# Performance work log

Hardware: AMD Instinct MI355X
Metric: run time of the kernel (lower is better)

Reference implementation:

```python
import jax, jax.numpy as jnp
import numpy as np

D_MODEL = 512
NUM_HEADS = 8
D_K = D_MODEL // NUM_HEADS
DIM_FF = 2048
EPS = 1e-5


def layer_norm(x, gamma, beta):
    mu = jnp.mean(x, axis=-1, keepdims=True)
    var = jnp.mean(jnp.square(x - mu), axis=-1, keepdims=True)
    return (x - mu) * jax.lax.rsqrt(var + EPS) * gamma + beta


def setup_inputs() -> dict:
    key = jax.random.key(0)
    ks = jax.random.split(key, 10)
    B, L = 8, 1024
    s = 1.0 / np.sqrt(D_MODEL)
    return {
        "h": jax.random.normal(ks[0], (B, L, D_MODEL), jnp.float32),
        "attn_bias": jax.random.normal(ks[1], (B, NUM_HEADS, L, L), jnp.float32),
        "mask": jnp.ones((B, L), jnp.int32),
        "Wqkv": jax.random.normal(ks[2], (D_MODEL, 3 * D_MODEL), jnp.float32) * s,
        "bqkv": jnp.zeros((3 * D_MODEL,), jnp.float32),
        "Wo": jax.random.normal(ks[3], (D_MODEL, D_MODEL), jnp.float32) * s,
        "bo": jnp.zeros((D_MODEL,), jnp.float32),
        "W1": jax.random.normal(ks[4], (D_MODEL, DIM_FF), jnp.float32) * s,
        "b1": jnp.zeros((DIM_FF,), jnp.float32),
        "W2": jax.random.normal(ks[5], (DIM_FF, D_MODEL), jnp.float32) * (1.0 / np.sqrt(DIM_FF)),
        "b2": jnp.zeros((D_MODEL,), jnp.float32),
        "g1": jnp.ones((D_MODEL,), jnp.float32),
        "be1": jnp.zeros((D_MODEL,), jnp.float32),
        "g2": jnp.ones((D_MODEL,), jnp.float32),
        "be2": jnp.zeros((D_MODEL,), jnp.float32),
    }


def reference(h, attn_bias, mask, Wqkv, bqkv, Wo, bo, W1, b1, W2, b2, g1, be1, g2, be2):
    B, L, D = h.shape
    H, dk = NUM_HEADS, D_K
    qkv = h @ Wqkv + bqkv                      # [B, L, 3D]
    q, k, v = jnp.split(qkv, 3, axis=-1)
    q = q.reshape(B, L, H, dk).transpose(0, 2, 1, 3)  # [B, H, L, dk]
    k = k.reshape(B, L, H, dk).transpose(0, 2, 1, 3)
    v = v.reshape(B, L, H, dk).transpose(0, 2, 1, 3)
    scores = jnp.einsum('bhqd,bhkd->bhqk', q, k) / np.sqrt(dk)
    scores = scores + attn_bias
    scores = jnp.where(mask[:, None, None, :] > 0, scores, -jnp.inf)
    attn = jax.nn.softmax(scores, axis=-1)
    out = jnp.einsum('bhqk,bhkd->bhqd', attn, v)       # [B, H, L, dk]
    out = out.transpose(0, 2, 1, 3).reshape(B, L, D)
    out = out @ Wo + bo
    h = layer_norm(h + out, g1, be1)
    ff = jax.nn.relu(h @ W1 + b1) @ W2 + b2
    h = layer_norm(h + ff, g2, be2)
    return h
```

## Files before the change

kernel.cpp:

```cpp
#include <hip/hip_runtime.h>
#include <hip/hip_bf16.h>
#include <math.h>

#define NUM_HEADS 8
#define SEQ_L 1024
#define EPS 1e-5f
#define KVBLK 64
#define LOG2E 1.44269504088896f

typedef __bf16 bf16x8 __attribute__((ext_vector_type(8)));
typedef float f32x4 __attribute__((ext_vector_type(4)));
typedef __hip_bfloat16 bf16;

#define AS1 __attribute__((address_space(1)))
#define AS3 __attribute__((address_space(3)))

__device__ __forceinline__ void gload_lds16(const void* g, void* l) {
    __builtin_amdgcn_global_load_lds((const AS1 unsigned*)g, (AS3 unsigned*)l, 16, 0, 0);
}

__device__ __forceinline__ unsigned short bfb(float x) {
    bf16 b = __float2bfloat16(x);
    return *(unsigned short*)&b;
}

__device__ __forceinline__ int swz64(int el, int row) { return el ^ ((row & 7) << 3); }

__global__ __launch_bounds__(256) void f32_to_bf16_kernel(
    const float* __restrict__ in, bf16* __restrict__ out, int n)
{
    const int i = (blockIdx.x * 256 + threadIdx.x) * 4;
    if (i >= n) return;
    const float4 v = *(const float4*)&in[i];
    out[i + 0] = __float2bfloat16(v.x);
    out[i + 1] = __float2bfloat16(v.y);
    out[i + 2] = __float2bfloat16(v.z);
    out[i + 3] = __float2bfloat16(v.w);
}

__global__ __launch_bounds__(256) void transpose_w(
    const float* __restrict__ W, bf16* __restrict__ Wt, int K, int N)
{
    __shared__ float t[32][33];
    const int tx = threadIdx.x & 31, ty = threadIdx.x >> 5;
    const int n0 = blockIdx.x * 32, k0 = blockIdx.y * 32;
    #pragma unroll
    for (int r = 0; r < 4; ++r)
        t[ty + 8 * r][tx] = W[(size_t)(k0 + ty + 8 * r) * N + n0 + tx];
    __syncthreads();
    #pragma unroll
    for (int r = 0; r < 4; ++r)
        Wt[(size_t)(n0 + ty + 8 * r) * K + k0 + tx] = __float2bfloat16(t[tx][ty + 8 * r]);
}

__global__ __launch_bounds__(256) void gemm_bf16(
    const bf16* __restrict__ A, const bf16* __restrict__ Bt,
    const float* __restrict__ bias,
    float* __restrict__ C, bf16* __restrict__ Cb,
    int M, int N, int K, int relu)
{
    __shared__ __align__(16) bf16 Abuf[128 * 32];
    __shared__ __align__(16) bf16 Bbuf[128 * 32];
    const int tid = threadIdx.x;
    const int wv = tid >> 6, lane = tid & 63;
    const int row0 = blockIdx.y * 128, col0 = blockIdx.x * 128;
    const int wm = (wv >> 1) * 64, wn = (wv & 1) * 64;
    const int r0 = lane & 15, kb = lane >> 4;

    f32x4 acc[4][4] = {};
    const int arow = lane >> 2;
    const int akoff = (lane & 3) * 8;

    for (int k0 = 0; k0 < K; k0 += 32) {
        #pragma unroll
        for (int s = 0; s < 2; ++s) {
            const int c = 2 * wv + s;
            gload_lds16(&A[(size_t)(row0 + c * 16 + arow) * K + k0 + akoff], &Abuf[c * 512]);
            gload_lds16(&Bt[(size_t)(col0 + c * 16 + arow) * K + k0 + akoff], &Bbuf[c * 512]);
        }
        __syncthreads();

        bf16x8 a[4], b[4];
        #pragma unroll
        for (int i = 0; i < 4; ++i)
            a[i] = *(const bf16x8*)&Abuf[(wm + i * 16 + r0) * 32 + kb * 8];
        #pragma unroll
        for (int j = 0; j < 4; ++j)
            b[j] = *(const bf16x8*)&Bbuf[(wn + j * 16 + r0) * 32 + kb * 8];
        #pragma unroll
        for (int i = 0; i < 4; ++i)
            #pragma unroll
            for (int j = 0; j < 4; ++j)
                acc[i][j] = __builtin_amdgcn_mfma_f32_16x16x32_bf16(a[i], b[j], acc[i][j], 0, 0, 0);
        __syncthreads();
    }

    float bv[4];
    #pragma unroll
    for (int j = 0; j < 4; ++j) bv[j] = bias[col0 + wn + j * 16 + r0];

    #pragma unroll
    for (int i = 0; i < 4; ++i) {
        #pragma unroll
        for (int j = 0; j < 4; ++j) {
            const int col = col0 + wn + j * 16 + r0;
            #pragma unroll
            for (int reg = 0; reg < 4; ++reg) {
                const int row = row0 + wm + i * 16 + kb * 4 + reg;
                float v = acc[i][j][reg] + bv[j];
                if (relu) v = fmaxf(v, 0.f);
                if (C)  C[(size_t)row * N + col] = v;
                if (Cb) Cb[(size_t)row * N + col] = __float2bfloat16(v);
            }
        }
    }
}

__global__ __launch_bounds__(256) void gemm_qkv(
    const bf16* __restrict__ A, const bf16* __restrict__ Bt,
    const float* __restrict__ bias,
    bf16* __restrict__ Qb, bf16* __restrict__ Kb, bf16* __restrict__ Vtb,
    int M, int N, int K)
{
    __shared__ __align__(16) bf16 Abuf[128 * 32];
    __shared__ __align__(16) bf16 Bbuf[128 * 32];
    const int tid = threadIdx.x;
    const int wv = tid >> 6, lane = tid & 63;
    const int row0 = blockIdx.y * 128, col0 = blockIdx.x * 128;
    const int wm = (wv >> 1) * 64, wn = (wv & 1) * 64;
    const int r0 = lane & 15, kb = lane >> 4;

    f32x4 acc[4][4] = {};
    const int arow = lane >> 2;
    const int akoff = (lane & 3) * 8;

    for (int k0 = 0; k0 < K; k0 += 32) {
        #pragma unroll
        for (int s = 0; s < 2; ++s) {
            const int c = 2 * wv + s;
            gload_lds16(&A[(size_t)(row0 + c * 16 + arow) * K + k0 + akoff], &Abuf[c * 512]);
            gload_lds16(&Bt[(size_t)(col0 + c * 16 + arow) * K + k0 + akoff], &Bbuf[c * 512]);
        }
        __syncthreads();

        bf16x8 a[4], b[4];
        #pragma unroll
        for (int i = 0; i < 4; ++i)
            a[i] = *(const bf16x8*)&Abuf[(wm + i * 16 + r0) * 32 + kb * 8];
        #pragma unroll
        for (int j = 0; j < 4; ++j)
            b[j] = *(const bf16x8*)&Bbuf[(wn + j * 16 + r0) * 32 + kb * 8];
        #pragma unroll
        for (int i = 0; i < 4; ++i)
            #pragma unroll
            for (int j = 0; j < 4; ++j)
                acc[i][j] = __builtin_amdgcn_mfma_f32_16x16x32_bf16(a[i], b[j], acc[i][j], 0, 0, 0);
        __syncthreads();
    }

    #pragma unroll
    for (int i = 0; i < 4; ++i) {
        #pragma unroll
        for (int j = 0; j < 4; ++j) {
            const int col = col0 + wn + j * 16 + r0;
            const float bv = bias[col];
            const int region = col >> 9;
            const int cc = col & 511;
            const int head = cc >> 6, d = cc & 63;
            const int l0 = row0 + wm + i * 16 + kb * 4;
            const int b_ = l0 >> 10, l_ = l0 & 1023;
            if (region == 2) {
                unsigned short pk[4];
                #pragma unroll
                for (int reg = 0; reg < 4; ++reg) pk[reg] = bfb(acc[i][j][reg] + bv);
                *(ushort4*)&Vtb[((size_t)(b_ * NUM_HEADS + head) * 64 + d) * SEQ_L + l_] =
                    make_ushort4(pk[0], pk[1], pk[2], pk[3]);
            } else {
                const float s = (region == 0) ? (0.125f * LOG2E) : 1.0f;
                bf16* dst = (region == 0) ? Qb : Kb;
                #pragma unroll
                for (int reg = 0; reg < 4; ++reg) {
                    dst[((size_t)(b_ * NUM_HEADS + head) * SEQ_L + l_ + reg) * 64 + d] =
                        __float2bfloat16((acc[i][j][reg] + bv) * s);
                }
            }
        }
    }
}

__global__ __launch_bounds__(256) void attn_mfma(
    const bf16* __restrict__ Qb, const bf16* __restrict__ Kb,
    const bf16* __restrict__ Vtb, const float* __restrict__ abias,
    const int* __restrict__ mask, bf16* __restrict__ out)
{
    const int bh = blockIdx.y;
    const int b = bh >> 3, h = bh & 7;
    const int q0 = blockIdx.x * 64;
    const int tid = threadIdx.x;
    const int wv = tid >> 6, lane = tid & 63;
    const int ql = lane & 15;
    const int hi = lane >> 4;

    __shared__ __align__(16) bf16 Ks[KVBLK * 64];
    __shared__ __align__(16) bf16 Vs[64 * KVBLK];
    __shared__ __align__(16) bf16 Ps[4][16 * 64];
    __shared__ __align__(16) float biasL[4][16 * 64];
    __shared__ float maskf[KVBLK];

    const int qrow = q0 + wv * 16 + ql;
    bf16x8 qf[2];
    #pragma unroll
    for (int kk = 0; kk < 2; ++kk)
        qf[kk] = *(const bf16x8*)&Qb[((size_t)bh * SEQ_L + qrow) * 64 + kk * 32 + hi * 8];

    const int sr = tid >> 3;
    const int sc8 = (tid & 7) * 8;
    const int br = lane >> 4;
    const int bc = (lane & 15) * 4;

    f32x4 o[4] = {};
    float m = -1e30f, l = 0.f;
    const size_t bias_base = ((size_t)(b * NUM_HEADS + h) * SEQ_L + q0 + wv * 16) * SEQ_L;

    bf16x8 kreg[2], vreg[2];
    f32x4 breg[4];
    float mreg = 0.f;
    #pragma unroll
    for (int it = 0; it < 2; ++it) {
        const int row = sr + it * 32;
        kreg[it] = *(const bf16x8*)&Kb[((size_t)bh * SEQ_L + row) * 64 + sc8];
        vreg[it] = *(const bf16x8*)&Vtb[((size_t)bh * 64 + row) * SEQ_L + sc8];
    }
    #pragma unroll
    for (int s = 0; s < 4; ++s)
        breg[s] = *(const f32x4*)&abias[bias_base + (size_t)(s * 4 + br) * SEQ_L + bc];
    if (tid < KVBLK) mreg = (mask[b * SEQ_L + tid] > 0) ? 0.f : -1e30f;

    for (int k0 = 0; k0 < SEQ_L; k0 += KVBLK) {
        __syncthreads();

        #pragma unroll
        for (int it = 0; it < 2; ++it) {
            const int row = sr + it * 32;
            *(bf16x8*)&Ks[swz64(row * 64 + sc8, row)] = kreg[it];
            *(bf16x8*)&Vs[swz64(row * 64 + sc8, row)] = vreg[it];
        }
        if (tid < KVBLK) maskf[tid] = mreg;
        #pragma unroll
        for (int s = 0; s < 4; ++s) {
            const int row = s * 4 + br;
            const int q = (bc >> 2) ^ (row & 7);
            *(f32x4*)&biasL[wv][row * 64 + q * 4] = breg[s];
        }
        __syncthreads();

        const int k1 = k0 + KVBLK;
        if (k1 < SEQ_L) {
            #pragma unroll
            for (int it = 0; it < 2; ++it) {
                const int row = sr + it * 32;
                kreg[it] = *(const bf16x8*)&Kb[((size_t)bh * SEQ_L + k1 + row) * 64 + sc8];
                vreg[it] = *(const bf16x8*)&Vtb[((size_t)bh * 64 + row) * SEQ_L + k1 + sc8];
            }
            #pragma unroll
            for (int s = 0; s < 4; ++s)
                breg[s] = *(const f32x4*)&abias[bias_base + (size_t)(s * 4 + br) * SEQ_L + k1 + bc];
            if (tid < KVBLK) mreg = (mask[b * SEQ_L + k1 + tid] > 0) ? 0.f : -1e30f;
        }

        f32x4 p[4];
        #pragma unroll
        for (int c = 0; c < 4; ++c) {
            const int q = (c * 4 + hi) ^ (ql & 7);
            const f32x4 bf = *(const f32x4*)&biasL[wv][ql * 64 + q * 4];
            const f32x4 mk = *(const f32x4*)&maskf[c * 16 + hi * 4];
            #pragma unroll
            for (int reg = 0; reg < 4; ++reg)
                p[c][reg] = fmaf(bf[reg], LOG2E, mk[reg]);
        }

        __builtin_amdgcn_s_setprio(1);
        #pragma unroll
        for (int c = 0; c < 4; ++c) {
            const int row = c * 16 + ql;
            #pragma unroll
            for (int kk = 0; kk < 2; ++kk) {
                bf16x8 kf = *(const bf16x8*)&Ks[swz64(row * 64 + kk * 32 + hi * 8, row)];
                p[c] = __builtin_amdgcn_mfma_f32_16x16x32_bf16(kf, qf[kk], p[c], 0, 0, 0);
            }
        }
        __builtin_amdgcn_s_setprio(0);

        float mx = p[0][0];
        #pragma unroll
        for (int c = 0; c < 4; ++c)
            #pragma unroll
            for (int reg = 0; reg < 4; ++reg) mx = fmaxf(mx, p[c][reg]);
        mx = fmaxf(mx, __shfl_xor(mx, 16, 64));
        mx = fmaxf(mx, __shfl_xor(mx, 32, 64));

        const float mnew = fmaxf(m, mx);
        const float scale = __builtin_exp2f(m - mnew);
        m = mnew;
        float lsum = 0.f;
        #pragma unroll
        for (int c = 0; c < 4; ++c)
            #pragma unroll
            for (int reg = 0; reg < 4; ++reg) {
                const float pv = __builtin_exp2f(p[c][reg] - mnew);
                p[c][reg] = pv;
                lsum += pv;
            }
        lsum += __shfl_xor(lsum, 16, 64);
        lsum += __shfl_xor(lsum, 32, 64);
        l = l * scale + lsum;

        #pragma unroll
        for (int c = 0; c < 4; ++c) {
            const int el = ql * 64 + c * 16 + hi * 4;
            uint2 pk;
            pk.x = (unsigned)bfb(p[c][0]) | ((unsigned)bfb(p[c][1]) << 16);
            pk.y = (unsigned)bfb(p[c][2]) | ((unsigned)bfb(p[c][3]) << 16);
            *(uint2*)&Ps[wv][swz64(el, ql)] = pk;
        }

        #pragma unroll
        for (int reg = 0; reg < 4; ++reg) {
            const float sc_q = __shfl(scale, (lane & 48) | (hi * 4 + reg), 64);
            #pragma unroll
            for (int c2 = 0; c2 < 4; ++c2) o[c2][reg] *= sc_q;
        }

        __builtin_amdgcn_s_setprio(1);
        #pragma unroll
        for (int kk = 0; kk < 2; ++kk) {
            bf16x8 pf = *(const bf16x8*)&Ps[wv][swz64(ql * 64 + kk * 32 + hi * 8, ql)];
            #pragma unroll
            for (int c2 = 0; c2 < 4; ++c2) {
                const int vrow = c2 * 16 + ql;
                bf16x8 vf = *(const bf16x8*)&Vs[swz64(vrow * 64 + kk * 32 + hi * 8, vrow)];
                o[c2] = __builtin_amdgcn_mfma_f32_16x16x32_bf16(pf, vf, o[c2], 0, 0, 0);
            }
        }
        __builtin_amdgcn_s_setprio(0);
    }

    const float invl = (l > 0.f) ? (1.0f / l) : 0.f;
    #pragma unroll
    for (int reg = 0; reg < 4; ++reg) {
        const float inv_q = __shfl(invl, (lane & 48) | (hi * 4 + reg), 64);
        const int row = q0 + wv * 16 + hi * 4 + reg;
        #pragma unroll
        for (int c2 = 0; c2 < 4; ++c2)
            out[((size_t)(b * SEQ_L + row)) * 512 + h * 64 + c2 * 16 + ql] =
                __float2bfloat16(o[c2][reg] * inv_q);
    }
}

__global__ __launch_bounds__(256) void add_ln_to_bf16(
    const float* __restrict__ X, const float* __restrict__ Y,
    const float* __restrict__ gamma, const float* __restrict__ beta,
    bf16* __restrict__ outb)
{
    const int wave = threadIdx.x >> 6;
    const int lane = threadIdx.x & 63;
    const int row = blockIdx.x * 4 + wave;
    const float* xp = X + (size_t)row * 512 + lane * 8;
    const float* yp = Y + (size_t)row * 512 + lane * 8;

    float v[8];
    const float4 a0 = *(const float4*)xp;
    const float4 a1 = *(const float4*)(xp + 4);
    const float4 b0 = *(const float4*)yp;
    const float4 b1 = *(const float4*)(yp + 4);
    v[0] = a0.x + b0.x; v[1] = a0.y + b0.y; v[2] = a0.z + b0.z; v[3] = a0.w + b0.w;
    v[4] = a1.x + b1.x; v[5] = a1.y + b1.y; v[6] = a1.z + b1.z; v[7] = a1.w + b1.w;

    float s = 0.f, sq = 0.f;
    #pragma unroll
    for (int i = 0; i < 8; ++i) { s += v[i]; sq += v[i] * v[i]; }
    #pragma unroll
    for (int off = 1; off < 64; off <<= 1) {
        s += __shfl_xor(s, off, 64);
        sq += __shfl_xor(sq, off, 64);
    }
    const float mu = s * (1.f / 512.f);
    const float var = sq * (1.f / 512.f) - mu * mu;
    const float rstd = rsqrtf(var + EPS);

    const int c = lane * 8;
    const float4 g0 = *(const float4*)&gamma[c];
    const float4 g1 = *(const float4*)&gamma[c + 4];
    const float4 e0 = *(const float4*)&beta[c];
    const float4 e1 = *(const float4*)&beta[c + 4];
    float r[8];
    r[0] = (v[0] - mu) * rstd * g0.x + e0.x;
    r[1] = (v[1] - mu) * rstd * g0.y + e0.y;
    r[2] = (v[2] - mu) * rstd * g0.z + e0.z;
    r[3] = (v[3] - mu) * rstd * g0.w + e0.w;
    r[4] = (v[4] - mu) * rstd * g1.x + e1.x;
    r[5] = (v[5] - mu) * rstd * g1.y + e1.y;
    r[6] = (v[6] - mu) * rstd * g1.z + e1.z;
    r[7] = (v[7] - mu) * rstd * g1.w + e1.w;

    uint4 w;
    w.x = (unsigned)bfb(r[0]) | ((unsigned)bfb(r[1]) << 16);
    w.y = (unsigned)bfb(r[2]) | ((unsigned)bfb(r[3]) << 16);
    w.z = (unsigned)bfb(r[4]) | ((unsigned)bfb(r[5]) << 16);
    w.w = (unsigned)bfb(r[6]) | ((unsigned)bfb(r[7]) << 16);
    *(uint4*)&outb[(size_t)row * 512 + c] = w;
}

__global__ __launch_bounds__(256) void add_ln_from_bf16(
    const bf16* __restrict__ Xb, const float* __restrict__ Y,
    const float* __restrict__ gamma, const float* __restrict__ beta,
    float* __restrict__ out)
{
    const int wave = threadIdx.x >> 6;
    const int lane = threadIdx.x & 63;
    const int row = blockIdx.x * 4 + wave;
    const bf16x8 xv = *(const bf16x8*)&Xb[(size_t)row * 512 + lane * 8];
    const float* yp = Y + (size_t)row * 512 + lane * 8;

    float v[8];
    const float4 b0 = *(const float4*)yp;
    const float4 b1 = *(const float4*)(yp + 4);
    v[0] = (float)xv[0] + b0.x; v[1] = (float)xv[1] + b0.y;
    v[2] = (float)xv[2] + b0.z; v[3] = (float)xv[3] + b0.w;
    v[4] = (float)xv[4] + b1.x; v[5] = (float)xv[5] + b1.y;
    v[6] = (float)xv[6] + b1.z; v[7] = (float)xv[7] + b1.w;

    float s = 0.f, sq = 0.f;
    #pragma unroll
    for (int i = 0; i < 8; ++i) { s += v[i]; sq += v[i] * v[i]; }
    #pragma unroll
    for (int off = 1; off < 64; off <<= 1) {
        s += __shfl_xor(s, off, 64);
        sq += __shfl_xor(sq, off, 64);
    }
    const float mu = s * (1.f / 512.f);
    const float var = sq * (1.f / 512.f) - mu * mu;
    const float rstd = rsqrtf(var + EPS);

    const int c = lane * 8;
    const float4 g0 = *(const float4*)&gamma[c];
    const float4 g1 = *(const float4*)&gamma[c + 4];
    const float4 e0 = *(const float4*)&beta[c];
    const float4 e1 = *(const float4*)&beta[c + 4];
    float4 r0, r1;
    r0.x = (v[0] - mu) * rstd * g0.x + e0.x;
    r0.y = (v[1] - mu) * rstd * g0.y + e0.y;
    r0.z = (v[2] - mu) * rstd * g0.z + e0.z;
    r0.w = (v[3] - mu) * rstd * g0.w + e0.w;
    r1.x = (v[4] - mu) * rstd * g1.x + e1.x;
    r1.y = (v[5] - mu) * rstd * g1.y + e1.y;
    r1.z = (v[6] - mu) * rstd * g1.z + e1.z;
    r1.w = (v[7] - mu) * rstd * g1.w + e1.w;
    float* op = out + (size_t)row * 512 + c;
    *(float4*)op = r0;
    *(float4*)(op + 4) = r1;
}

extern "C" void kernel_launch(void* const* d_in, const int* in_sizes, int n_in,
                              void* d_out, int out_size, void* d_ws, size_t ws_size,
                              hipStream_t stream)
{
    const float* h    = (const float*)d_in[0];
    const float* ab   = (const float*)d_in[1];
    const int*   mask = (const int*)d_in[2];
    const float* Wqkv = (const float*)d_in[3];
    const float* bqkv = (const float*)d_in[4];
    const float* Wo   = (const float*)d_in[5];
    const float* bo   = (const float*)d_in[6];
    const float* W1   = (const float*)d_in[7];
    const float* b1   = (const float*)d_in[8];
    const float* W2   = (const float*)d_in[9];
    const float* b2   = (const float*)d_in[10];
    const float* g1   = (const float*)d_in[11];
    const float* be1  = (const float*)d_in[12];
    const float* g2   = (const float*)d_in[13];
    const float* be2  = (const float*)d_in[14];
    float* out = (float*)d_out;
    char* ws = (char*)d_ws;

    const int M = 8 * 1024;
    const size_t MB = 1024 * 1024;

    bf16*  hb   = (bf16*)(ws + 0 * MB);
    bf16*  Wtq  = (bf16*)(ws + 8 * MB);
    bf16*  Wto  = (bf16*)(ws + 10 * MB);
    bf16*  Wt1  = (bf16*)(ws + 11 * MB);
    bf16*  Wt2  = (bf16*)(ws + 13 * MB);
    bf16*  Qb   = (bf16*)(ws + 15 * MB);
    bf16*  Kb   = (bf16*)(ws + 23 * MB);
    bf16*  Vtb  = (bf16*)(ws + 31 * MB);
    bf16*  aob  = (bf16*)(ws + 39 * MB);
    float* proj = (float*)(ws + 47 * MB);
    bf16*  h1b  = (bf16*)(ws + 63 * MB);
    bf16*  ffb  = (bf16*)(ws + 71 * MB);
    float* f2   = (float*)(ws + 15 * MB);

    f32_to_bf16_kernel<<<dim3(M * 512 / 1024), 256, 0, stream>>>(h, hb, M * 512);
    transpose_w<<<dim3(1536 / 32, 512 / 32), 256, 0, stream>>>(Wqkv, Wtq, 512, 1536);
    transpose_w<<<dim3(512 / 32, 512 / 32), 256, 0, stream>>>(Wo, Wto, 512, 512);
    transpose_w<<<dim3(2048 / 32, 512 / 32), 256, 0, stream>>>(W1, Wt1, 512, 2048);
    transpose_w<<<dim3(512 / 32, 2048 / 32), 256, 0, stream>>>(W2, Wt2, 2048, 512);

    gemm_qkv<<<dim3(1536 / 128, M / 128), 256, 0, stream>>>(hb, Wtq, bqkv, Qb, Kb, Vtb, M, 1536, 512);
    attn_mfma<<<dim3(SEQ_L / 64, 64), 256, 0, stream>>>(Qb, Kb, Vtb, ab, mask, aob);
    gemm_bf16<<<dim3(512 / 128, M / 128), 256, 0, stream>>>(aob, Wto, bo, proj, nullptr, M, 512, 512, 0);
    add_ln_to_bf16<<<dim3(M / 4), 256, 0, stream>>>(h, proj, g1, be1, h1b);
    gemm_bf16<<<dim3(2048 / 128, M / 128), 256, 0, stream>>>(h1b, Wt1, b1, nullptr, ffb, M, 2048, 512, 1);
    gemm_bf16<<<dim3(512 / 128, M / 128), 256, 0, stream>>>(ffb, Wt2, b2, f2, nullptr, M, 512, 2048, 0);
    add_ln_from_bf16<<<dim3(M / 4), 256, 0, stream>>>(h1b, f2, g2, be2, out);
}
```

Measured before the change: 265.7 us.

## Merge prep kernels, store GEMM outputs in bf16, read K/V directly in attention

Five conversion and transpose launches become one prep_kernel that dispatches on block index. The Wo and W2 GEMMs now write bf16 instead of fp32, halving their output traffic and the matching layer-norm reads. The attention kernel drops its LDS staging and register prefetch of K, V, bias and mask. It reads them straight from global memory or cache with no block barriers and requests 4 blocks per CU. This risks uncoalesced, unpipelined global reads in the attention inner loop and some precision loss on the residual inputs.

```diff
diff --git a/kernel.cpp b/kernel.cpp
--- a/kernel.cpp
+++ b/kernel.cpp
@@ -26,37 +26,49 @@
 
 __device__ __forceinline__ int swz64(int el, int row) { return el ^ ((row & 7) << 3); }
 
-__global__ __launch_bounds__(256) void f32_to_bf16_kernel(
-    const float* __restrict__ in, bf16* __restrict__ out, int n)
-{
-    const int i = (blockIdx.x * 256 + threadIdx.x) * 4;
-    if (i >= n) return;
-    const float4 v = *(const float4*)&in[i];
-    out[i + 0] = __float2bfloat16(v.x);
-    out[i + 1] = __float2bfloat16(v.y);
-    out[i + 2] = __float2bfloat16(v.z);
-    out[i + 3] = __float2bfloat16(v.w);
-}
-
-__global__ __launch_bounds__(256) void transpose_w(
-    const float* __restrict__ W, bf16* __restrict__ Wt, int K, int N)
-{
+__global__ __launch_bounds__(256) void prep_kernel(
+    const float* __restrict__ h, const float* __restrict__ Wqkv,
+    const float* __restrict__ Wo, const float* __restrict__ W1,
+    const float* __restrict__ W2,
+    bf16* __restrict__ hb, bf16* __restrict__ Wtq, bf16* __restrict__ Wto,
+    bf16* __restrict__ Wt1, bf16* __restrict__ Wt2)
+{
+    const int bid = blockIdx.x;
+    const int tid = threadIdx.x;
+    if (bid < 2048) {
+        const int i = (bid * 256 + tid) * 8;
+        const float4 v0 = *(const float4*)&h[i];
+        const float4 v1 = *(const float4*)&h[i + 4];
+        uint4 w;
+        w.x = (unsigned)bfb(v0.x) | ((unsigned)bfb(v0.y) << 16);
+        w.y = (unsigned)bfb(v0.z) | ((unsigned)bfb(v0.w) << 16);
+        w.z = (unsigned)bfb(v1.x) | ((unsigned)bfb(v1.y) << 16);
+        w.w = (unsigned)bfb(v1.z) | ((unsigned)bfb(v1.w) << 16);
+        *(uint4*)&hb[i] = w;
+        return;
+    }
+    int r = bid - 2048;
+    const float* W; bf16* Wt; int K, N, bx, by;
+    if (r < 768)        { W = Wqkv; Wt = Wtq; K = 512;  N = 1536; bx = r % 48; by = r / 48; }
+    else if (r < 1024)  { r -= 768;  W = Wo; Wt = Wto; K = 512;  N = 512;  bx = r % 16; by = r / 16; }
+    else if (r < 2048)  { r -= 1024; W = W1; Wt = Wt1; K = 512;  N = 2048; bx = r % 64; by = r / 64; }
+    else                { r -= 2048; W = W2; Wt = Wt2; K = 2048; N = 512;  bx = r % 16; by = r / 16; }
+
     __shared__ float t[32][33];
-    const int tx = threadIdx.x & 31, ty = threadIdx.x >> 5;
-    const int n0 = blockIdx.x * 32, k0 = blockIdx.y * 32;
-    #pragma unroll
-    for (int r = 0; r < 4; ++r)
-        t[ty + 8 * r][tx] = W[(size_t)(k0 + ty + 8 * r) * N + n0 + tx];
+    const int tx = tid & 31, ty = tid >> 5;
+    const int n0 = bx * 32, k0 = by * 32;
+    #pragma unroll
+    for (int q = 0; q < 4; ++q)
+        t[ty + 8 * q][tx] = W[(size_t)(k0 + ty + 8 * q) * N + n0 + tx];
     __syncthreads();
     #pragma unroll
-    for (int r = 0; r < 4; ++r)
-        Wt[(size_t)(n0 + ty + 8 * r) * K + k0 + tx] = __float2bfloat16(t[tx][ty + 8 * r]);
+    for (int q = 0; q < 4; ++q)
+        Wt[(size_t)(n0 + ty + 8 * q) * K + k0 + tx] = __float2bfloat16(t[tx][ty + 8 * q]);
 }
 
 __global__ __launch_bounds__(256) void gemm_bf16(
     const bf16* __restrict__ A, const bf16* __restrict__ Bt,
-    const float* __restrict__ bias,
-    float* __restrict__ C, bf16* __restrict__ Cb,
+    const float* __restrict__ bias, bf16* __restrict__ Cb,
     int M, int N, int K, int relu)
 {
     __shared__ __align__(16) bf16 Abuf[128 * 32];
@@ -109,8 +121,7 @@
                 const int row = row0 + wm + i * 16 + kb * 4 + reg;
                 float v = acc[i][j][reg] + bv[j];
                 if (relu) v = fmaxf(v, 0.f);
-                if (C)  C[(size_t)row * N + col] = v;
-                if (Cb) Cb[(size_t)row * N + col] = __float2bfloat16(v);
+                Cb[(size_t)row * N + col] = __float2bfloat16(v);
             }
         }
     }
@@ -188,104 +199,52 @@
     }
 }
 
-__global__ __launch_bounds__(256) void attn_mfma(
+__global__ __launch_bounds__(256, 4) void attn_mfma(
     const bf16* __restrict__ Qb, const bf16* __restrict__ Kb,
     const bf16* __restrict__ Vtb, const float* __restrict__ abias,
     const int* __restrict__ mask, bf16* __restrict__ out)
 {
     const int bh = blockIdx.y;
     const int b = bh >> 3, h = bh & 7;
-    const int q0 = blockIdx.x * 64;
     const int tid = threadIdx.x;
     const int wv = tid >> 6, lane = tid & 63;
     const int ql = lane & 15;
     const int hi = lane >> 4;
-
-    __shared__ __align__(16) bf16 Ks[KVBLK * 64];
-    __shared__ __align__(16) bf16 Vs[64 * KVBLK];
+    const int q0 = blockIdx.x * 64 + wv * 16;
+
     __shared__ __align__(16) bf16 Ps[4][16 * 64];
-    __shared__ __align__(16) float biasL[4][16 * 64];
-    __shared__ float maskf[KVBLK];
-
-    const int qrow = q0 + wv * 16 + ql;
+
+    const int qrow = q0 + ql;
     bf16x8 qf[2];
     #pragma unroll
     for (int kk = 0; kk < 2; ++kk)
         qf[kk] = *(const bf16x8*)&Qb[((size_t)bh * SEQ_L + qrow) * 64 + kk * 32 + hi * 8];
 
-    const int sr = tid >> 3;
-    const int sc8 = (tid & 7) * 8;
-    const int br = lane >> 4;
-    const int bc = (lane & 15) * 4;
-
     f32x4 o[4] = {};
     float m = -1e30f, l = 0.f;
-    const size_t bias_base = ((size_t)(b * NUM_HEADS + h) * SEQ_L + q0 + wv * 16) * SEQ_L;
-
-    bf16x8 kreg[2], vreg[2];
-    f32x4 breg[4];
-    float mreg = 0.f;
-    #pragma unroll
-    for (int it = 0; it < 2; ++it) {
-        const int row = sr + it * 32;
-        kreg[it] = *(const bf16x8*)&Kb[((size_t)bh * SEQ_L + row) * 64 + sc8];
-        vreg[it] = *(const bf16x8*)&Vtb[((size_t)bh * 64 + row) * SEQ_L + sc8];
-    }
-    #pragma unroll
-    for (int s = 0; s < 4; ++s)
-        breg[s] = *(const f32x4*)&abias[bias_base + (size_t)(s * 4 + br) * SEQ_L + bc];
-    if (tid < KVBLK) mreg = (mask[b * SEQ_L + tid] > 0) ? 0.f : -1e30f;
+    const size_t bias_row = ((size_t)(b * NUM_HEADS + h) * SEQ_L + qrow) * SEQ_L;
+    const bf16* Kbase = Kb + (size_t)bh * SEQ_L * 64;
+    const bf16* Vbase = Vtb + (size_t)bh * 64 * SEQ_L;
+    const int* mbase = mask + b * SEQ_L;
 
     for (int k0 = 0; k0 < SEQ_L; k0 += KVBLK) {
-        __syncthreads();
-
-        #pragma unroll
-        for (int it = 0; it < 2; ++it) {
-            const int row = sr + it * 32;
-            *(bf16x8*)&Ks[swz64(row * 64 + sc8, row)] = kreg[it];
-            *(bf16x8*)&Vs[swz64(row * 64 + sc8, row)] = vreg[it];
-        }
-        if (tid < KVBLK) maskf[tid] = mreg;
-        #pragma unroll
-        for (int s = 0; s < 4; ++s) {
-            const int row = s * 4 + br;
-            const int q = (bc >> 2) ^ (row & 7);
-            *(f32x4*)&biasL[wv][row * 64 + q * 4] = breg[s];
-        }
-        __syncthreads();
-
-        const int k1 = k0 + KVBLK;
-        if (k1 < SEQ_L) {
-            #pragma unroll
-            for (int it = 0; it < 2; ++it) {
-                const int row = sr + it * 32;
-                kreg[it] = *(const bf16x8*)&Kb[((size_t)bh * SEQ_L + k1 + row) * 64 + sc8];
-                vreg[it] = *(const bf16x8*)&Vtb[((size_t)bh * 64 + row) * SEQ_L + k1 + sc8];
-            }
-            #pragma unroll
-            for (int s = 0; s < 4; ++s)
-                breg[s] = *(const f32x4*)&abias[bias_base + (size_t)(s * 4 + br) * SEQ_L + k1 + bc];
-            if (tid < KVBLK) mreg = (mask[b * SEQ_L + k1 + tid] > 0) ? 0.f : -1e30f;
-        }
-
         f32x4 p[4];
         #pragma unroll
         for (int c = 0; c < 4; ++c) {
-            const int q = (c * 4 + hi) ^ (ql & 7);
-            const f32x4 bf = *(const f32x4*)&biasL[wv][ql * 64 + q * 4];
-            const f32x4 mk = *(const f32x4*)&maskf[c * 16 + hi * 4];
-            #pragma unroll
-            for (int reg = 0; reg < 4; ++reg)
-                p[c][reg] = fmaf(bf[reg], LOG2E, mk[reg]);
+            const f32x4 b4 = *(const f32x4*)&abias[bias_row + k0 + c * 16 + hi * 4];
+            const int4 m4 = *(const int4*)&mbase[k0 + c * 16 + hi * 4];
+            p[c][0] = (m4.x > 0) ? b4[0] * LOG2E : -1e30f;
+            p[c][1] = (m4.y > 0) ? b4[1] * LOG2E : -1e30f;
+            p[c][2] = (m4.z > 0) ? b4[2] * LOG2E : -1e30f;
+            p[c][3] = (m4.w > 0) ? b4[3] * LOG2E : -1e30f;
         }
 
         __builtin_amdgcn_s_setprio(1);
         #pragma unroll
         for (int c = 0; c < 4; ++c) {
-            const int row = c * 16 + ql;
             #pragma unroll
             for (int kk = 0; kk < 2; ++kk) {
-                bf16x8 kf = *(const bf16x8*)&Ks[swz64(row * 64 + kk * 32 + hi * 8, row)];
+                const bf16x8 kf = *(const bf16x8*)&Kbase[(size_t)(k0 + c * 16 + ql) * 64 + kk * 32 + hi * 8];
                 p[c] = __builtin_amdgcn_mfma_f32_16x16x32_bf16(kf, qf[kk], p[c], 0, 0, 0);
             }
         }
@@ -334,11 +293,10 @@
         __builtin_amdgcn_s_setprio(1);
         #pragma unroll
         for (int kk = 0; kk < 2; ++kk) {
-            bf16x8 pf = *(const bf16x8*)&Ps[wv][swz64(ql * 64 + kk * 32 + hi * 8, ql)];
+            const bf16x8 pf = *(const bf16x8*)&Ps[wv][swz64(ql * 64 + kk * 32 + hi * 8, ql)];
             #pragma unroll
             for (int c2 = 0; c2 < 4; ++c2) {
-                const int vrow = c2 * 16 + ql;
-                bf16x8 vf = *(const bf16x8*)&Vs[swz64(vrow * 64 + kk * 32 + hi * 8, vrow)];
+                const bf16x8 vf = *(const bf16x8*)&Vbase[(size_t)(c2 * 16 + ql) * SEQ_L + k0 + kk * 32 + hi * 8];
                 o[c2] = __builtin_amdgcn_mfma_f32_16x16x32_bf16(pf, vf, o[c2], 0, 0, 0);
             }
         }
@@ -349,7 +307,7 @@
     #pragma unroll
     for (int reg = 0; reg < 4; ++reg) {
         const float inv_q = __shfl(invl, (lane & 48) | (hi * 4 + reg), 64);
-        const int row = q0 + wv * 16 + hi * 4 + reg;
+        const int row = q0 + hi * 4 + reg;
         #pragma unroll
         for (int c2 = 0; c2 < 4; ++c2)
             out[((size_t)(b * SEQ_L + row)) * 512 + h * 64 + c2 * 16 + ql] =
@@ -358,7 +316,7 @@
 }
 
 __global__ __launch_bounds__(256) void add_ln_to_bf16(
-    const float* __restrict__ X, const float* __restrict__ Y,
+    const float* __restrict__ X, const bf16* __restrict__ Yb,
     const float* __restrict__ gamma, const float* __restrict__ beta,
     bf16* __restrict__ outb)
 {
@@ -366,15 +324,15 @@
     const int lane = threadIdx.x & 63;
     const int row = blockIdx.x * 4 + wave;
     const float* xp = X + (size_t)row * 512 + lane * 8;
-    const float* yp = Y + (size_t)row * 512 + lane * 8;
+    const bf16x8 yv = *(const bf16x8*)&Yb[(size_t)row * 512 + lane * 8];
 
     float v[8];
     const float4 a0 = *(const float4*)xp;
     const float4 a1 = *(const float4*)(xp + 4);
-    const float4 b0 = *(const float4*)yp;
-    const float4 b1 = *(const float4*)(yp + 4);
-    v[0] = a0.x + b0.x; v[1] = a0.y + b0.y; v[2] = a0.z + b0.z; v[3] = a0.w + b0.w;
-    v[4] = a1.x + b1.x; v[5] = a1.y + b1.y; v[6] = a1.z + b1.z; v[7] = a1.w + b1.w;
+    v[0] = a0.x + (float)yv[0]; v[1] = a0.y + (float)yv[1];
+    v[2] = a0.z + (float)yv[2]; v[3] = a0.w + (float)yv[3];
+    v[4] = a1.x + (float)yv[4]; v[5] = a1.y + (float)yv[5];
+    v[6] = a1.z + (float)yv[6]; v[7] = a1.w + (float)yv[7];
 
     float s = 0.f, sq = 0.f;
     #pragma unroll
@@ -412,7 +370,7 @@
 }
 
 __global__ __launch_bounds__(256) void add_ln_from_bf16(
-    const bf16* __restrict__ Xb, const float* __restrict__ Y,
+    const bf16* __restrict__ Xb, const bf16* __restrict__ Yb,
     const float* __restrict__ gamma, const float* __restrict__ beta,
     float* __restrict__ out)
 {
@@ -420,15 +378,11 @@
     const int lane = threadIdx.x & 63;
     const int row = blockIdx.x * 4 + wave;
     const bf16x8 xv = *(const bf16x8*)&Xb[(size_t)row * 512 + lane * 8];
-    const float* yp = Y + (size_t)row * 512 + lane * 8;
+    const bf16x8 yv = *(const bf16x8*)&Yb[(size_t)row * 512 + lane * 8];
 
     float v[8];
-    const float4 b0 = *(const float4*)yp;
-    const float4 b1 = *(const float4*)(yp + 4);
-    v[0] = (float)xv[0] + b0.x; v[1] = (float)xv[1] + b0.y;
-    v[2] = (float)xv[2] + b0.z; v[3] = (float)xv[3] + b0.w;
-    v[4] = (float)xv[4] + b1.x; v[5] = (float)xv[5] + b1.y;
-    v[6] = (float)xv[6] + b1.z; v[7] = (float)xv[7] + b1.w;
+    #pragma unroll
+    for (int i = 0; i < 8; ++i) v[i] = (float)xv[i] + (float)yv[i];
 
     float s = 0.f, sq = 0.f;
     #pragma unroll
@@ -486,31 +440,26 @@
     const int M = 8 * 1024;
     const size_t MB = 1024 * 1024;
 
-    bf16*  hb   = (bf16*)(ws + 0 * MB);
-    bf16*  Wtq  = (bf16*)(ws + 8 * MB);
-    bf16*  Wto  = (bf16*)(ws + 10 * MB);
-    bf16*  Wt1  = (bf16*)(ws + 11 * MB);
-    bf16*  Wt2  = (bf16*)(ws + 13 * MB);
-    bf16*  Qb   = (bf16*)(ws + 15 * MB);
-    bf16*  Kb   = (bf16*)(ws + 23 * MB);
-    bf16*  Vtb  = (bf16*)(ws + 31 * MB);
-    bf16*  aob  = (bf16*)(ws + 39 * MB);
-    float* proj = (float*)(ws + 47 * MB);
-    bf16*  h1b  = (bf16*)(ws + 63 * MB);
-    bf16*  ffb  = (bf16*)(ws + 71 * MB);
-    float* f2   = (float*)(ws + 15 * MB);
-
-    f32_to_bf16_kernel<<<dim3(M * 512 / 1024), 256, 0, stream>>>(h, hb, M * 512);
-    transpose_w<<<dim3(1536 / 32, 512 / 32), 256, 0, stream>>>(Wqkv, Wtq, 512, 1536);
-    transpose_w<<<dim3(512 / 32, 512 / 32), 256, 0, stream>>>(Wo, Wto, 512, 512);
-    transpose_w<<<dim3(2048 / 32, 512 / 32), 256, 0, stream>>>(W1, Wt1, 512, 2048);
-    transpose_w<<<dim3(512 / 32, 2048 / 32), 256, 0, stream>>>(W2, Wt2, 2048, 512);
-
+    bf16*  hb    = (bf16*)(ws + 0 * MB);
+    bf16*  Wtq   = (bf16*)(ws + 8 * MB);
+    bf16*  Wto   = (bf16*)(ws + 10 * MB);
+    bf16*  Wt1   = (bf16*)(ws + 11 * MB);
+    bf16*  Wt2   = (bf16*)(ws + 13 * MB);
+    bf16*  Qb    = (bf16*)(ws + 15 * MB);
+    bf16*  Kb    = (bf16*)(ws + 23 * MB);
+    bf16*  Vtb   = (bf16*)(ws + 31 * MB);
+    bf16*  aob   = (bf16*)(ws + 39 * MB);
+    bf16*  projb = (bf16*)(ws + 47 * MB);
+    bf16*  h1b   = (bf16*)(ws + 55 * MB);
+    bf16*  ffb   = (bf16*)(ws + 63 * MB);
+    bf16*  f2b   = (bf16*)(ws + 95 * MB);
+
+    prep_kernel<<<dim3(5120), 256, 0, stream>>>(h, Wqkv, Wo, W1, W2, hb, Wtq, Wto, Wt1, Wt2);
     gemm_qkv<<<dim3(1536 / 128, M / 128), 256, 0, stream>>>(hb, Wtq, bqkv, Qb, Kb, Vtb, M, 1536, 512);
     attn_mfma<<<dim3(SEQ_L / 64, 64), 256, 0, stream>>>(Qb, Kb, Vtb, ab, mask, aob);
-    gemm_bf16<<<dim3(512 / 128, M / 128), 256, 0, stream>>>(aob, Wto, bo, proj, nullptr, M, 512, 512, 0);
-    add_ln_to_bf16<<<dim3(M / 4), 256, 0, stream>>>(h, proj, g1, be1, h1b);
-    gemm_bf16<<<dim3(2048 / 128, M / 128), 256, 0, stream>>>(h1b, Wt1, b1, nullptr, ffb, M, 2048, 512, 1);
-    gemm_bf16<<<dim3(512 / 128, M / 128), 256, 0, stream>>>(ffb, Wt2, b2, f2, nullptr, M, 512, 2048, 0);
-    add_ln_from_bf16<<<dim3(M / 4), 256, 0, stream>>>(h1b, f2, g2, be2, out);
-}
+    gemm_bf16<<<dim3(512 / 128, M / 128), 256, 0, stream>>>(aob, Wto, bo, projb, M, 512, 512, 0);
+    add_ln_to_bf16<<<dim3(M / 4), 256, 0, stream>>>(h, projb, g1, be1, h1b);
+    gemm_bf16<<<dim3(2048 / 128, M / 128), 256, 0, stream>>>(h1b, Wt1, b1, ffb, M, 2048, 512, 1);
+    gemm_bf16<<<dim3(512 / 128, M / 128), 256, 0, stream>>>(ffb, Wt2, b2, f2b, M, 512, 2048, 0);
+    add_ln_from_bf16<<<dim3(M / 4), 256, 0, stream>>>(h1b, f2b, g2, be2, out);
+}
```

Result: slower. 326.8 us (+23.0%).
